# Kernel optimization log

Hardware: AMD Instinct MI355X
Metric: run time of the kernel (lower is better)

Reference implementation:

```python
import jax, jax.numpy as jnp
import numpy as np

FIRE_RATE = 0.5  # from init_kwargs
TOTAL_C = 16     # hidden_channels + 1


def _perception_filters(C, dtype):
    # Faithful to reg_perception_filters (including the sobel_x entries as written).
    identity = jnp.array([[0.0, 0.0, 0.0], [0.0, 1.0, 0.0], [0.0, 0.0, 0.0]], dtype=dtype)
    sobel_x = jnp.array([[1.0, 0.0, 1.0], [2.0, 0.0, -2.0], [1.0, 0.0, -1.0]], dtype=dtype) / 8.0
    sobel_y = jnp.array([[1.0, 2.0, 1.0], [0.0, 0.0, 0.0], [-1.0, -2.0, -1.0]], dtype=dtype) / 8.0
    f = jnp.stack([identity, sobel_x, sobel_y])[:, None, :, :]  # [3,1,3,3]
    # Grouped depthwise conv: each input channel -> 3 outputs, ordered
    # [ch0_id, ch0_sx, ch0_sy, ch1_id, ...] matching the torch per-channel cat.
    return jnp.tile(f, (C, 1, 1, 1))  # [3C,1,3,3]


def setup_inputs() -> dict:
    key = jax.random.key(0)
    k1, k2, k3, k4, k5, k6 = jax.random.split(key, 6)
    B, C, H, W = 32, TOTAL_C, 256, 256
    P = 3 * C  # perception channels = 48
    return {
        "grid": jax.random.normal(k1, (B, C, H, W), dtype=jnp.float32),
        "noise": jax.random.normal(k2, (B, 1, H, W), dtype=jnp.float32),
        "w1": jax.random.normal(k3, (128, P), dtype=jnp.float32) * 0.05,
        "b1": jax.random.normal(k4, (128,), dtype=jnp.float32) * 0.05,
        "w2": jax.random.normal(k5, (C, 128), dtype=jnp.float32) * 0.05,
        "b2": jax.random.normal(k6, (C,), dtype=jnp.float32) * 0.05,
    }


def reference(grid, noise, w1, b1, w2, b2):
    B, C, H, W = grid.shape
    filt = _perception_filters(C, grid.dtype)  # [3C,1,3,3]
    # Per-channel identity/sobel stencil as one grouped depthwise conv.
    perception = jax.lax.conv_general_dilated(
        grid, filt, window_strides=(1, 1), padding="SAME",
        dimension_numbers=("NCHW", "OIHW", "NCHW"), feature_group_count=C,
    )  # [B,3C,H,W]
    # update_net: 1x1 conv -> ReLU -> 1x1 conv (expressed as channel GEMMs)
    h = jax.nn.relu(jnp.einsum("oc,bchw->bohw", w1, perception) + b1[None, :, None, None])
    update = jnp.einsum("oc,bchw->bohw", w2, h) + b2[None, :, None, None]
    # stochastic mask: (randn < fire_rate), broadcast over channels
    mask = (noise < FIRE_RATE).astype(grid.dtype)
    return jnp.clip(grid + update * mask, -2.0, 2.0)
```

## Files before the change

kernel.cpp:

```cpp
#include <hip/hip_runtime.h>

#define NC   16
#define NP   48
#define NH   128
#define HDIM 256
#define WDIM 256
#define HW   (HDIM*WDIM)

#define PSTR  48
#define HSTR  136
#define W2STR 136

typedef __attribute__((ext_vector_type(8))) short short8;
typedef __attribute__((ext_vector_type(4))) float f32x4;
typedef __attribute__((ext_vector_type(4))) int   int4v;

__device__ __forceinline__ unsigned cvt_pk(float lo, float hi) {
    unsigned r;
    asm("v_cvt_pk_bf16_f32 %0, %1, %2" : "=v"(r) : "v"(lo), "v"(hi));
    return r;
}

__global__ __launch_bounds__(256, 4) void nca_mfma_kernel(
    const float* __restrict__ grid,
    const float* __restrict__ noise,
    const float* __restrict__ w1,
    const float* __restrict__ b1,
    const float* __restrict__ w2,
    const float* __restrict__ b2,
    float* __restrict__ out)
{
    __shared__ short sW1F[8 * 768];
    __shared__ short sP[HDIM * PSTR];

    short* w2s = sP;
    float* sS  = (float*)&sP[10736];

    const int tid  = threadIdx.x;
    const int b    = blockIdx.x >> 8;
    const int y    = blockIdx.x & 255;
    const int wv   = tid >> 6;
    const int lane = tid & 63;
    const int q    = lane >> 4;
    const int l15  = lane & 15;

    {
        const int o = tid >> 1, half = tid & 1;
        const float* src = w1 + o * NP + 24 * half;
        const int n = o >> 4, r15 = o & 15;
        #pragma unroll
        for (int g = 0; g < 3; ++g) {
            const int k0 = 24 * half + 8 * g;
            const int tt = k0 >> 5, qq = (k0 & 31) >> 3;
            unsigned u0 = cvt_pk(src[8*g+0], src[8*g+1]);
            unsigned u1 = cvt_pk(src[8*g+2], src[8*g+3]);
            unsigned u2 = cvt_pk(src[8*g+4], src[8*g+5]);
            unsigned u3 = cvt_pk(src[8*g+6], src[8*g+7]);
            int4v v = {(int)u0, (int)u1, (int)u2, (int)u3};
            *(int4v*)&sW1F[n*768 + (tt ? 512 : 0) + (qq*16 + r15)*8] = v;
        }
        const int j = tid >> 4, seg = tid & 15;
        const float* s2 = w2 + j * NH + seg * 8;
        unsigned v0 = cvt_pk(s2[0], s2[1]), v1 = cvt_pk(s2[2], s2[3]);
        unsigned v2 = cvt_pk(s2[4], s2[5]), v3 = cvt_pk(s2[6], s2[7]);
        int4v vv = {(int)v0, (int)v1, (int)v2, (int)v3};
        *(int4v*)&w2s[j * W2STR + seg * 8] = vv;
        if (tid < 3) { sS[tid*258 + 256] = 0.f; sS[tid*258 + 257] = 0.f; }
    }
    __syncthreads();

    short8 w2f[4];
    #pragma unroll
    for (int t = 0; t < 4; ++t) {
        short8 v;
        #pragma unroll
        for (int jj = 0; jj < 8; ++jj) v[jj] = w2s[l15 * W2STR + jj*16 + 4*t + q];
        w2f[t] = v;
    }
    float b1v[8];
    #pragma unroll
    for (int n = 0; n < 8; ++n) b1v[n] = b1[16*n + l15];
    const float b2v = b2[l15];

    const int  x   = tid;
    const bool ld  = (tid < 192);
    const int  r   = tid >> 6, seg = tid & 63;
    int rowY = y - 1 + r; rowY = rowY < 0 ? 0 : (rowY > 255 ? 255 : rowY);
    const bool zr = (r == 0 && y == 0) || (r == 2 && y == 255);
    const float* gp = grid + (size_t)b * NC * HW + (size_t)rowY * WDIM + 4 * seg;

    float4 v0 = {0.f, 0.f, 0.f, 0.f};
    if (ld) { v0 = *(const float4*)gp; gp += HW; if (zr) { float4 z = {0,0,0,0}; v0 = z; } }
    if (ld) *(float4*)&sS[r*258 + 4*seg] = v0;
    __syncthreads();

    const int xl = x ? (x - 1) : 256;
    const int xr = (x < 255) ? (x + 1) : 256;

    unsigned pk[24];
    float carry = 0.f;
    #pragma unroll
    for (int c = 0; c < 16; ++c) {
        float4 vn = {0.f, 0.f, 0.f, 0.f};
        if (ld && c < 15) { vn = *(const float4*)gp; gp += HW; if (zr) { float4 z = {0,0,0,0}; vn = z; } }

        const float tl = sS[xl],       tm = sS[x],       tr = sS[xr];
        const float ml = sS[258 + xl], mm = sS[258 + x], mr = sS[258 + xr];
        const float bl = sS[516 + xl], bm = sS[516 + x], br = sS[516 + xr];
        const float p1 = (tl + tr + 2.f*ml - 2.f*mr + bl - br) * 0.125f;
        const float p2 = (tl + 2.f*tm + tr - bl - 2.f*bm - br) * 0.125f;
        if (c & 1) { pk[(3*c - 1) / 2] = cvt_pk(carry, mm); pk[(3*c + 1) / 2] = cvt_pk(p1, p2); }
        else       { pk[3*c / 2]       = cvt_pk(mm, p1);    carry = p2; }

        __syncthreads();
        if (ld && c < 15) *(float4*)&sS[r*258 + 4*seg] = vn;
        __syncthreads();
    }

    {
        short* row = &sP[x * PSTR];
        #pragma unroll
        for (int i = 0; i < 6; ++i) {
            int4v v = {(int)pk[4*i], (int)pk[4*i+1], (int)pk[4*i+2], (int)pk[4*i+3]};
            *(int4v*)&row[8*i] = v;
        }
    }
    __syncthreads();

    short8 aF0[3], aF1[3];
    #pragma unroll
    for (int m = 1; m < 4; ++m) {
        const short* pr = &sP[((wv*4 + m)*16 + l15) * PSTR];
        aF0[m-1] = *(const short8*)&pr[8*q];
        short8 a1 = {};
        if (q < 2) a1 = *(const short8*)&pr[32 + 8*q];
        aF1[m-1] = a1;
    }
    short* Hb = &sP[(wv*64 + 16) * PSTR];

    #pragma unroll
    for (int mt = 0; mt < 4; ++mt) {
        short8 a0, a1;
        if (mt == 0) {
            const short* pr = &sP[(wv*64 + l15) * PSTR];
            a0 = *(const short8*)&pr[8*q];
            short8 z = {}; a1 = z;
            if (q < 2) a1 = *(const short8*)&pr[32 + 8*q];
        } else { a0 = aF0[mt-1]; a1 = aF1[mt-1]; }

        f32x4 acc[8];
        #pragma unroll
        for (int n = 0; n < 8; ++n) { f32x4 t4 = {b1v[n], b1v[n], b1v[n], b1v[n]}; acc[n] = t4; }
        #pragma unroll
        for (int n = 0; n < 8; ++n) {
            const short8 bf0 = *(const short8*)&sW1F[n*768 + lane*8];
            acc[n] = __builtin_amdgcn_mfma_f32_16x16x32_bf16(a0, bf0, acc[n], 0, 0, 0);
        }
        #pragma unroll
        for (int n = 0; n < 8; ++n) {
            short8 bf1 = {};
            if (lane < 32) bf1 = *(const short8*)&sW1F[n*768 + 512 + lane*8];
            acc[n] = __builtin_amdgcn_mfma_f32_16x16x32_bf16(a1, bf1, acc[n], 0, 0, 0);
        }

        #pragma unroll
        for (int rr = 0; rr < 4; ++rr) {
            unsigned h0 = cvt_pk(fmaxf(acc[0][rr], 0.f), fmaxf(acc[1][rr], 0.f));
            unsigned h1 = cvt_pk(fmaxf(acc[2][rr], 0.f), fmaxf(acc[3][rr], 0.f));
            unsigned h2 = cvt_pk(fmaxf(acc[4][rr], 0.f), fmaxf(acc[5][rr], 0.f));
            unsigned h3 = cvt_pk(fmaxf(acc[6][rr], 0.f), fmaxf(acc[7][rr], 0.f));
            int4v v = {(int)h0, (int)h1, (int)h2, (int)h3};
            *(int4v*)&Hb[(q*4 + rr) * HSTR + l15 * 8] = v;
        }
        f32x4 acc2 = {b2v, b2v, b2v, b2v};
        #pragma unroll
        for (int t = 0; t < 4; ++t) {
            const short8 af = *(const short8*)&Hb[l15 * HSTR + 32*t + 8*q];
            acc2 = __builtin_amdgcn_mfma_f32_16x16x32_bf16(af, w2f[t], acc2, 0, 0, 0);
        }
        const int px0 = (wv*4 + mt) * 16;
        const int px  = px0 + 4*q;
        const size_t gi = (size_t)b * NC * HW + (size_t)l15 * HW + (size_t)y * WDIM + px;
        const float4 g  = *(const float4*)&grid[gi];
        const float4 nz = *(const float4*)&noise[(size_t)b * HW + (size_t)y * WDIM + px];
        float4 o;
        o.x = fminf(fmaxf(g.x + acc2[0] * (nz.x < 0.5f ? 1.f : 0.f), -2.f), 2.f);
        o.y = fminf(fmaxf(g.y + acc2[1] * (nz.y < 0.5f ? 1.f : 0.f), -2.f), 2.f);
        o.z = fminf(fmaxf(g.z + acc2[2] * (nz.z < 0.5f ? 1.f : 0.f), -2.f), 2.f);
        o.w = fminf(fmaxf(g.w + acc2[3] * (nz.w < 0.5f ? 1.f : 0.f), -2.f), 2.f);
        *(float4*)&out[gi] = o;
    }
}

extern "C" void kernel_launch(void* const* d_in, const int* in_sizes, int n_in,
                              void* d_out, int out_size, void* d_ws, size_t ws_size,
                              hipStream_t stream) {
    const float* grid  = (const float*)d_in[0];
    const float* noise = (const float*)d_in[1];
    const float* w1    = (const float*)d_in[2];
    const float* b1    = (const float*)d_in[3];
    const float* w2    = (const float*)d_in[4];
    const float* b2    = (const float*)d_in[5];
    float* out = (float*)d_out;

    dim3 g(32 * 256);
    nca_mfma_kernel<<<g, 256, 0, stream>>>(grid, noise, w1, b1, w2, b2, out);
}
```

Baseline: 449.0 us.

## Batch-load halo rows into bf16 LDS, drop per-channel barriers, swizzle block order

The per-channel stencil loop, which used double barriers and a ring buffer, is replaced. All 48 row-channel float4 loads are now issued up front into registers, converted to bf16 and written to LDS once, and the stencil is computed from LDS without further syncs. W2 is read straight from global memory with software bf16 rounding instead of being staged in LDS. The block index is remapped so that concurrently scheduled blocks cover distant rows, and the output uses nontemporal stores. The trade-off is that stencil inputs are rounded to bf16 before the Sobel sums, which lowers precision, and holding 12 float4 values per thread raises register pressure.

Measured after the change: 457.6 us. About the same (+1.9%).

```diff
diff --git a/kernel.cpp b/kernel.cpp
--- a/kernel.cpp
+++ b/kernel.cpp
@@ -7,18 +7,26 @@
 #define WDIM 256
 #define HW   (HDIM*WDIM)
 
-#define PSTR  48
-#define HSTR  136
-#define W2STR 136
+#define PSTR 48
+#define HSTR 136
 
 typedef __attribute__((ext_vector_type(8))) short short8;
 typedef __attribute__((ext_vector_type(4))) float f32x4;
 typedef __attribute__((ext_vector_type(4))) int   int4v;
+typedef __attribute__((ext_vector_type(2))) int   int2v;
 
 __device__ __forceinline__ unsigned cvt_pk(float lo, float hi) {
     unsigned r;
     asm("v_cvt_pk_bf16_f32 %0, %1, %2" : "=v"(r) : "v"(lo), "v"(hi));
     return r;
+}
+__device__ __forceinline__ short f2bf(float f) {
+    unsigned u = __float_as_uint(f);
+    u += 0x7FFFu + ((u >> 16) & 1u);
+    return (short)(u >> 16);
+}
+__device__ __forceinline__ float b2f(short s) {
+    return __uint_as_float((unsigned)(unsigned short)s << 16);
 }
 
 __global__ __launch_bounds__(256, 4) void nca_mfma_kernel(
@@ -33,12 +41,12 @@
     __shared__ short sW1F[8 * 768];
     __shared__ short sP[HDIM * PSTR];
 
-    short* w2s = sP;
-    float* sS  = (float*)&sP[10736];
-
     const int tid  = threadIdx.x;
-    const int b    = blockIdx.x >> 8;
-    const int y    = blockIdx.x & 255;
+    const int id   = blockIdx.x;
+    const int k    = id >> 3;
+    const int b    = k >> 5;
+    const int y    = (id & 7) * 32 + (k & 31);
+
     const int wv   = tid >> 6;
     const int lane = tid & 63;
     const int q    = lane >> 4;
@@ -59,22 +67,27 @@
             int4v v = {(int)u0, (int)u1, (int)u2, (int)u3};
             *(int4v*)&sW1F[n*768 + (tt ? 512 : 0) + (qq*16 + r15)*8] = v;
         }
-        const int j = tid >> 4, seg = tid & 15;
-        const float* s2 = w2 + j * NH + seg * 8;
-        unsigned v0 = cvt_pk(s2[0], s2[1]), v1 = cvt_pk(s2[2], s2[3]);
-        unsigned v2 = cvt_pk(s2[4], s2[5]), v3 = cvt_pk(s2[6], s2[7]);
-        int4v vv = {(int)v0, (int)v1, (int)v2, (int)v3};
-        *(int4v*)&w2s[j * W2STR + seg * 8] = vv;
-        if (tid < 3) { sS[tid*258 + 256] = 0.f; sS[tid*258 + 257] = 0.f; }
-    }
-    __syncthreads();
+    }
+
+    float4 vbuf[12];
+    {
+        const int seg = tid & 63;
+        const size_t gbase = (size_t)b * NC * HW + 4 * seg;
+        #pragma unroll
+        for (int j = 0; j < 12; ++j) {
+            const int rc = wv + 4*j;
+            const int row = rc >> 4, ch = rc & 15;
+            int ry = y - 1 + row; ry = ry < 0 ? 0 : (ry > 255 ? 255 : ry);
+            vbuf[j] = *(const float4*)(grid + gbase + (size_t)ch * HW + (size_t)ry * WDIM);
+        }
+    }
 
     short8 w2f[4];
     #pragma unroll
     for (int t = 0; t < 4; ++t) {
         short8 v;
         #pragma unroll
-        for (int jj = 0; jj < 8; ++jj) v[jj] = w2s[l15 * W2STR + jj*16 + 4*t + q];
+        for (int jj = 0; jj < 8; ++jj) v[jj] = f2bf(w2[l15 * NH + jj*16 + 4*t + q]);
         w2f[t] = v;
     }
     float b1v[8];
@@ -82,47 +95,50 @@
     for (int n = 0; n < 8; ++n) b1v[n] = b1[16*n + l15];
     const float b2v = b2[l15];
 
-    const int  x   = tid;
-    const bool ld  = (tid < 192);
-    const int  r   = tid >> 6, seg = tid & 63;
-    int rowY = y - 1 + r; rowY = rowY < 0 ? 0 : (rowY > 255 ? 255 : rowY);
-    const bool zr = (r == 0 && y == 0) || (r == 2 && y == 255);
-    const float* gp = grid + (size_t)b * NC * HW + (size_t)rowY * WDIM + 4 * seg;
-
-    float4 v0 = {0.f, 0.f, 0.f, 0.f};
-    if (ld) { v0 = *(const float4*)gp; gp += HW; if (zr) { float4 z = {0,0,0,0}; v0 = z; } }
-    if (ld) *(float4*)&sS[r*258 + 4*seg] = v0;
+    {
+        const int seg = tid & 63;
+        #pragma unroll
+        for (int j = 0; j < 12; ++j) {
+            const int rc = wv + 4*j, row = rc >> 4;
+            float4 v = vbuf[j];
+            const bool zr = (row == 0 && y == 0) || (row == 2 && y == 255);
+            if (zr) { float4 z = {0,0,0,0}; v = z; }
+            int2v pv = {(int)cvt_pk(v.x, v.y), (int)cvt_pk(v.z, v.w)};
+            *(int2v*)&sP[rc * 256 + seg * 4] = pv;
+        }
+    }
     __syncthreads();
 
-    const int xl = x ? (x - 1) : 256;
-    const int xr = (x < 255) ? (x + 1) : 256;
-
     unsigned pk[24];
-    float carry = 0.f;
-    #pragma unroll
-    for (int c = 0; c < 16; ++c) {
-        float4 vn = {0.f, 0.f, 0.f, 0.f};
-        if (ld && c < 15) { vn = *(const float4*)gp; gp += HW; if (zr) { float4 z = {0,0,0,0}; vn = z; } }
-
-        const float tl = sS[xl],       tm = sS[x],       tr = sS[xr];
-        const float ml = sS[258 + xl], mm = sS[258 + x], mr = sS[258 + xr];
-        const float bl = sS[516 + xl], bm = sS[516 + x], br = sS[516 + xr];
-        const float p1 = (tl + tr + 2.f*ml - 2.f*mr + bl - br) * 0.125f;
-        const float p2 = (tl + 2.f*tm + tr - bl - 2.f*bm - br) * 0.125f;
-        if (c & 1) { pk[(3*c - 1) / 2] = cvt_pk(carry, mm); pk[(3*c + 1) / 2] = cvt_pk(p1, p2); }
-        else       { pk[3*c / 2]       = cvt_pk(mm, p1);    carry = p2; }
-
-        __syncthreads();
-        if (ld && c < 15) *(float4*)&sS[r*258 + 4*seg] = vn;
-        __syncthreads();
-    }
-
-    {
-        short* row = &sP[x * PSTR];
+    {
+        const int x = tid;
+        const bool xm = (x > 0), xp = (x < 255);
+        const int xl = xm ? x - 1 : 0;
+        const int xr = xp ? x + 1 : 255;
+        float carry = 0.f;
+        #pragma unroll
+        for (int c = 0; c < 16; ++c) {
+            const short* bT = &sP[c * 256];
+            const float tl0 = b2f(bT[xl]),        tm = b2f(bT[x]),        tr0 = b2f(bT[xr]);
+            const float ml0 = b2f(bT[4096 + xl]), mm = b2f(bT[4096 + x]), mr0 = b2f(bT[4096 + xr]);
+            const float bl0 = b2f(bT[8192 + xl]), bm = b2f(bT[8192 + x]), br0 = b2f(bT[8192 + xr]);
+            const float tl = xm ? tl0 : 0.f, tr = xp ? tr0 : 0.f;
+            const float ml = xm ? ml0 : 0.f, mr = xp ? mr0 : 0.f;
+            const float bl = xm ? bl0 : 0.f, br = xp ? br0 : 0.f;
+            const float p1 = (tl + tr + 2.f*ml - 2.f*mr + bl - br) * 0.125f;
+            const float p2 = (tl + 2.f*tm + tr - bl - 2.f*bm - br) * 0.125f;
+            if (c & 1) { pk[(3*c - 1) / 2] = cvt_pk(carry, mm); pk[(3*c + 1) / 2] = cvt_pk(p1, p2); }
+            else       { pk[3*c / 2]       = cvt_pk(mm, p1);    carry = p2; }
+        }
+    }
+    __syncthreads();
+
+    {
+        short* rowp = &sP[tid * PSTR];
         #pragma unroll
         for (int i = 0; i < 6; ++i) {
             int4v v = {(int)pk[4*i], (int)pk[4*i+1], (int)pk[4*i+2], (int)pk[4*i+3]};
-            *(int4v*)&row[8*i] = v;
+            *(int4v*)&rowp[8*i] = v;
         }
     }
     __syncthreads();
@@ -183,12 +199,12 @@
         const size_t gi = (size_t)b * NC * HW + (size_t)l15 * HW + (size_t)y * WDIM + px;
         const float4 g  = *(const float4*)&grid[gi];
         const float4 nz = *(const float4*)&noise[(size_t)b * HW + (size_t)y * WDIM + px];
-        float4 o;
-        o.x = fminf(fmaxf(g.x + acc2[0] * (nz.x < 0.5f ? 1.f : 0.f), -2.f), 2.f);
-        o.y = fminf(fmaxf(g.y + acc2[1] * (nz.y < 0.5f ? 1.f : 0.f), -2.f), 2.f);
-        o.z = fminf(fmaxf(g.z + acc2[2] * (nz.z < 0.5f ? 1.f : 0.f), -2.f), 2.f);
-        o.w = fminf(fmaxf(g.w + acc2[3] * (nz.w < 0.5f ? 1.f : 0.f), -2.f), 2.f);
-        *(float4*)&out[gi] = o;
+        f32x4 o;
+        o[0] = fminf(fmaxf(g.x + acc2[0] * (nz.x < 0.5f ? 1.f : 0.f), -2.f), 2.f);
+        o[1] = fminf(fmaxf(g.y + acc2[1] * (nz.y < 0.5f ? 1.f : 0.f), -2.f), 2.f);
+        o[2] = fminf(fmaxf(g.z + acc2[2] * (nz.z < 0.5f ? 1.f : 0.f), -2.f), 2.f);
+        o[3] = fminf(fmaxf(g.w + acc2[3] * (nz.w < 0.5f ? 1.f : 0.f), -2.f), 2.f);
+        __builtin_nontemporal_store(o, (f32x4*)&out[gi]);
     }
 }
 
```

## Compute stencil from direct global loads per wave, swizzle perception LDS, hoist weights

Applied to the files above, without the earlier changes.

Replaces the 16-iteration shared-memory row rotation, which needed two barriers per channel, with each wave loading three rows of four channels straight from global memory and computing the stencil in registers. The perception tile in LDS gets an XOR swizzle to reduce bank conflicts, and the block order is remapped so consecutive blocks cover different rows. W1 fragments are hoisted into registers once instead of being reloaded from LDS in each tile iteration, and W2 is converted straight from global memory. In exchange it issues redundant halo loads from global memory and uses more registers, which could lower occupancy.

Result: slower. 784.8 us (+74.8%).

```diff
diff --git a/kernel.cpp b/kernel.cpp
--- a/kernel.cpp
+++ b/kernel.cpp
@@ -7,18 +7,37 @@
 #define WDIM 256
 #define HW   (HDIM*WDIM)
 
-#define PSTR  48
-#define HSTR  136
-#define W2STR 136
+#define PSTR 48
+#define HSTR 136
 
 typedef __attribute__((ext_vector_type(8))) short short8;
 typedef __attribute__((ext_vector_type(4))) float f32x4;
 typedef __attribute__((ext_vector_type(4))) int   int4v;
+typedef __attribute__((ext_vector_type(2))) int   int2v;
 
 __device__ __forceinline__ unsigned cvt_pk(float lo, float hi) {
     unsigned r;
     asm("v_cvt_pk_bf16_f32 %0, %1, %2" : "=v"(r) : "v"(lo), "v"(hi));
     return r;
+}
+__device__ __forceinline__ short f2bf(float f) {
+    unsigned u = __float_as_uint(f);
+    u += 0x7FFFu + ((u >> 16) & 1u);
+    return (short)(u >> 16);
+}
+
+__device__ __forceinline__ int2v* spb(short* sP, int px, int off) {
+    int byte = px * 96 + off;
+    byte ^= ((px >> 2) & 15) << 3;
+    return (int2v*)((char*)sP + byte);
+}
+__device__ __forceinline__ short8 ld_sp16(short* sP, int px, int off) {
+    int2v lo = *spb(sP, px, off);
+    int2v hi = *spb(sP, px, off + 8);
+    union { int4v i; short8 s; } u;
+    int4v c = {lo[0], lo[1], hi[0], hi[1]};
+    u.i = c;
+    return u.s;
 }
 
 __global__ __launch_bounds__(256, 4) void nca_mfma_kernel(
@@ -33,12 +52,12 @@
     __shared__ short sW1F[8 * 768];
     __shared__ short sP[HDIM * PSTR];
 
-    short* w2s = sP;
-    float* sS  = (float*)&sP[10736];
-
     const int tid  = threadIdx.x;
-    const int b    = blockIdx.x >> 8;
-    const int y    = blockIdx.x & 255;
+    const int id   = blockIdx.x;
+    const int kk   = id >> 3;
+    const int b    = kk >> 5;
+    const int y    = (id & 7) * 32 + (kk & 31);
+
     const int wv   = tid >> 6;
     const int lane = tid & 63;
     const int q    = lane >> 4;
@@ -59,22 +78,74 @@
             int4v v = {(int)u0, (int)u1, (int)u2, (int)u3};
             *(int4v*)&sW1F[n*768 + (tt ? 512 : 0) + (qq*16 + r15)*8] = v;
         }
-        const int j = tid >> 4, seg = tid & 15;
-        const float* s2 = w2 + j * NH + seg * 8;
-        unsigned v0 = cvt_pk(s2[0], s2[1]), v1 = cvt_pk(s2[2], s2[3]);
-        unsigned v2 = cvt_pk(s2[4], s2[5]), v3 = cvt_pk(s2[6], s2[7]);
-        int4v vv = {(int)v0, (int)v1, (int)v2, (int)v3};
-        *(int4v*)&w2s[j * W2STR + seg * 8] = vv;
-        if (tid < 3) { sS[tid*258 + 256] = 0.f; sS[tid*258 + 257] = 0.f; }
+    }
+
+    {
+        const bool zT = (y == 0), zB = (y == 255);
+        const size_t rT = (size_t)(zT ? y : y - 1) * WDIM;
+        const size_t rM = (size_t)y * WDIM;
+        const size_t rB = (size_t)(zB ? y : y + 1) * WDIM;
+        const float* cbase = grid + (size_t)b * NC * HW + (size_t)(4 * wv) * HW;
+        const int xel = lane ? 4*lane - 1 : 0;
+        const int xer = (lane < 63) ? 4*lane + 4 : 255;
+
+        unsigned d[4][6];
+        float carry[4];
+        #pragma unroll
+        for (int c2 = 0; c2 < 4; ++c2) {
+            const float* pc = cbase + (size_t)c2 * HW;
+            f32x4 vT = *(const f32x4*)&pc[rT + 4*lane];
+            f32x4 vM = *(const f32x4*)&pc[rM + 4*lane];
+            f32x4 vB = *(const f32x4*)&pc[rB + 4*lane];
+            float eTl = pc[rT + xel], eMl = pc[rM + xel], eBl = pc[rB + xel];
+            float eTr = pc[rT + xer], eMr = pc[rM + xer], eBr = pc[rB + xer];
+            if (zT) { f32x4 z = {0,0,0,0}; vT = z; eTl = 0.f; eTr = 0.f; }
+            if (zB) { f32x4 z = {0,0,0,0}; vB = z; eBl = 0.f; eBr = 0.f; }
+            if (lane == 0)  { eTl = 0.f; eMl = 0.f; eBl = 0.f; }
+            if (lane == 63) { eTr = 0.f; eMr = 0.f; eBr = 0.f; }
+            #pragma unroll
+            for (int i = 0; i < 4; ++i) {
+                const float tl = i ? vT[i-1] : eTl;
+                const float tr = (i < 3) ? vT[i+1] : eTr;
+                const float ml = i ? vM[i-1] : eMl;
+                const float mr = (i < 3) ? vM[i+1] : eMr;
+                const float bl = i ? vB[i-1] : eBl;
+                const float br = (i < 3) ? vB[i+1] : eBr;
+                const float p0 = vM[i];
+                const float p1 = (tl + tr + 2.f*ml - 2.f*mr + bl - br) * 0.125f;
+                const float p2 = (tl + 2.f*vT[i] + tr - bl - 2.f*vB[i] - br) * 0.125f;
+                if (c2 == 0)      { d[i][0] = cvt_pk(p0, p1);       carry[i] = p2; }
+                else if (c2 == 1) { d[i][1] = cvt_pk(carry[i], p0); d[i][2] = cvt_pk(p1, p2); }
+                else if (c2 == 2) { d[i][3] = cvt_pk(p0, p1);       carry[i] = p2; }
+                else              { d[i][4] = cvt_pk(carry[i], p0); d[i][5] = cvt_pk(p1, p2); }
+            }
+        }
+        #pragma unroll
+        for (int i = 0; i < 4; ++i) {
+            const int px = 4*lane + i;
+            int2v v0 = {(int)d[i][0], (int)d[i][1]};
+            int2v v1 = {(int)d[i][2], (int)d[i][3]};
+            int2v v2 = {(int)d[i][4], (int)d[i][5]};
+            *spb(sP, px, 24*wv + 0)  = v0;
+            *spb(sP, px, 24*wv + 8)  = v1;
+            *spb(sP, px, 24*wv + 16) = v2;
+        }
     }
     __syncthreads();
 
+    short8 w1f0[8], w1f1[8];
+    #pragma unroll
+    for (int n = 0; n < 8; ++n) {
+        w1f0[n] = *(const short8*)&sW1F[n*768 + lane*8];
+        short8 z = {}; w1f1[n] = z;
+        if (lane < 32) w1f1[n] = *(const short8*)&sW1F[n*768 + 512 + lane*8];
+    }
     short8 w2f[4];
     #pragma unroll
     for (int t = 0; t < 4; ++t) {
         short8 v;
         #pragma unroll
-        for (int jj = 0; jj < 8; ++jj) v[jj] = w2s[l15 * W2STR + jj*16 + 4*t + q];
+        for (int jj = 0; jj < 8; ++jj) v[jj] = f2bf(w2[l15 * NH + jj*16 + 4*t + q]);
         w2f[t] = v;
     }
     float b1v[8];
@@ -82,58 +153,13 @@
     for (int n = 0; n < 8; ++n) b1v[n] = b1[16*n + l15];
     const float b2v = b2[l15];
 
-    const int  x   = tid;
-    const bool ld  = (tid < 192);
-    const int  r   = tid >> 6, seg = tid & 63;
-    int rowY = y - 1 + r; rowY = rowY < 0 ? 0 : (rowY > 255 ? 255 : rowY);
-    const bool zr = (r == 0 && y == 0) || (r == 2 && y == 255);
-    const float* gp = grid + (size_t)b * NC * HW + (size_t)rowY * WDIM + 4 * seg;
-
-    float4 v0 = {0.f, 0.f, 0.f, 0.f};
-    if (ld) { v0 = *(const float4*)gp; gp += HW; if (zr) { float4 z = {0,0,0,0}; v0 = z; } }
-    if (ld) *(float4*)&sS[r*258 + 4*seg] = v0;
-    __syncthreads();
-
-    const int xl = x ? (x - 1) : 256;
-    const int xr = (x < 255) ? (x + 1) : 256;
-
-    unsigned pk[24];
-    float carry = 0.f;
-    #pragma unroll
-    for (int c = 0; c < 16; ++c) {
-        float4 vn = {0.f, 0.f, 0.f, 0.f};
-        if (ld && c < 15) { vn = *(const float4*)gp; gp += HW; if (zr) { float4 z = {0,0,0,0}; vn = z; } }
-
-        const float tl = sS[xl],       tm = sS[x],       tr = sS[xr];
-        const float ml = sS[258 + xl], mm = sS[258 + x], mr = sS[258 + xr];
-        const float bl = sS[516 + xl], bm = sS[516 + x], br = sS[516 + xr];
-        const float p1 = (tl + tr + 2.f*ml - 2.f*mr + bl - br) * 0.125f;
-        const float p2 = (tl + 2.f*tm + tr - bl - 2.f*bm - br) * 0.125f;
-        if (c & 1) { pk[(3*c - 1) / 2] = cvt_pk(carry, mm); pk[(3*c + 1) / 2] = cvt_pk(p1, p2); }
-        else       { pk[3*c / 2]       = cvt_pk(mm, p1);    carry = p2; }
-
-        __syncthreads();
-        if (ld && c < 15) *(float4*)&sS[r*258 + 4*seg] = vn;
-        __syncthreads();
-    }
-
-    {
-        short* row = &sP[x * PSTR];
-        #pragma unroll
-        for (int i = 0; i < 6; ++i) {
-            int4v v = {(int)pk[4*i], (int)pk[4*i+1], (int)pk[4*i+2], (int)pk[4*i+3]};
-            *(int4v*)&row[8*i] = v;
-        }
-    }
-    __syncthreads();
-
     short8 aF0[3], aF1[3];
     #pragma unroll
     for (int m = 1; m < 4; ++m) {
-        const short* pr = &sP[((wv*4 + m)*16 + l15) * PSTR];
-        aF0[m-1] = *(const short8*)&pr[8*q];
+        const int px = (wv*4 + m)*16 + l15;
+        aF0[m-1] = ld_sp16(sP, px, 16*q);
         short8 a1 = {};
-        if (q < 2) a1 = *(const short8*)&pr[32 + 8*q];
+        if (q < 2) a1 = ld_sp16(sP, px, 64 + 16*q);
         aF1[m-1] = a1;
     }
     short* Hb = &sP[(wv*64 + 16) * PSTR];
@@ -142,26 +168,21 @@
     for (int mt = 0; mt < 4; ++mt) {
         short8 a0, a1;
         if (mt == 0) {
-            const short* pr = &sP[(wv*64 + l15) * PSTR];
-            a0 = *(const short8*)&pr[8*q];
+            const int px = wv*64 + l15;
+            a0 = ld_sp16(sP, px, 16*q);
             short8 z = {}; a1 = z;
-            if (q < 2) a1 = *(const short8*)&pr[32 + 8*q];
+            if (q < 2) a1 = ld_sp16(sP, px, 64 + 16*q);
         } else { a0 = aF0[mt-1]; a1 = aF1[mt-1]; }
 
         f32x4 acc[8];
         #pragma unroll
         for (int n = 0; n < 8; ++n) { f32x4 t4 = {b1v[n], b1v[n], b1v[n], b1v[n]}; acc[n] = t4; }
         #pragma unroll
-        for (int n = 0; n < 8; ++n) {
-            const short8 bf0 = *(const short8*)&sW1F[n*768 + lane*8];
-            acc[n] = __builtin_amdgcn_mfma_f32_16x16x32_bf16(a0, bf0, acc[n], 0, 0, 0);
-        }
-        #pragma unroll
-        for (int n = 0; n < 8; ++n) {
-            short8 bf1 = {};
-            if (lane < 32) bf1 = *(const short8*)&sW1F[n*768 + 512 + lane*8];
-            acc[n] = __builtin_amdgcn_mfma_f32_16x16x32_bf16(a1, bf1, acc[n], 0, 0, 0);
-        }
+        for (int n = 0; n < 8; ++n)
+            acc[n] = __builtin_amdgcn_mfma_f32_16x16x32_bf16(a0, w1f0[n], acc[n], 0, 0, 0);
+        #pragma unroll
+        for (int n = 0; n < 8; ++n)
+            acc[n] = __builtin_amdgcn_mfma_f32_16x16x32_bf16(a1, w1f1[n], acc[n], 0, 0, 0);
 
         #pragma unroll
         for (int rr = 0; rr < 4; ++rr) {
```
